# Kernel optimization log

Hardware: AMD Instinct MI355X
Metric: run time of the kernel (lower is better)

The kernel has to match this reference:

```python
import jax, jax.numpy as jnp
import numpy as np

B, T, D = 32, 1024, 512
MAX_LEN = 8192


def setup_inputs() -> dict:
    key = jax.random.key(0)
    k1, k2 = jax.random.split(key)
    x = jax.random.normal(k1, (B, T, D), dtype=jnp.float32)
    duration = jax.random.randint(k2, (B, T), 0, 8, dtype=jnp.int64)
    return {"x": x, "duration": duration, "max_len": MAX_LEN}


def reference(x, duration, max_len):
    # Length regulator: repeat each token vector x[b, i] duration[b, i] times,
    # then zero-pad each batch row to max_len.
    # Equivalent vectorized form: output index j maps to the source token i
    # such that cumsum(duration)[i-1] <= j < cumsum(duration)[i].
    cum = jnp.cumsum(duration, axis=1)                      # [B, T]
    mel_len = cum[:, -1]                                    # [B]
    pos = jnp.arange(max_len)                               # [L]
    # idx[b, j] = searchsorted_right(cum[b], j)
    idx = jax.vmap(lambda c: jnp.searchsorted(c, pos, side="right"))(cum)  # [B, L]
    idx = jnp.minimum(idx, x.shape[1] - 1)
    out = jnp.take_along_axis(x, idx[:, :, None], axis=1)   # [B, L, D]
    mask = (pos[None, :] < mel_len[:, None]).astype(x.dtype)  # [B, L]
    out = out * mask[:, :, None]                            # zero padding region
    return out, mel_len
```

## Files before the change

### kernel.cpp

```cpp
#include <hip/hip_runtime.h>
#include <stdint.h>

#define B_      32
#define T_      1024
#define D_      512
#define MAXLEN_ 8192

typedef float f4 __attribute__((ext_vector_type(4)));

__global__ void lr_scan_idx_kernel(const int* __restrict__ dur,
                                   int* __restrict__ idx,
                                   float* __restrict__ mel_out) {
    int b = blockIdx.x;
    int t = threadIdx.x;
    __shared__ int s[T_];
    s[t] = dur[b * T_ + t];
    __syncthreads();
    #pragma unroll
    for (int off = 1; off < T_; off <<= 1) {
        int v = (t >= off) ? s[t - off] : 0;
        __syncthreads();
        s[t] += v;
        __syncthreads();
    }
    int mel = s[T_ - 1];
    if (t == T_ - 1) {
        mel_out[b] = (float)mel;
    }
    #pragma unroll
    for (int k = 0; k < MAXLEN_ / T_; ++k) {
        int p = t + k * T_;
        int r = -1;
        if (p < mel) {
            int lo = 0, hi = T_;
            #pragma unroll
            for (int it = 0; it < 10; ++it) {
                int mid = (lo + hi) >> 1;
                if (s[mid] <= p) lo = mid + 1; else hi = mid;
            }
            r = lo;
        }
        idx[b * MAXLEN_ + p] = r;
    }
}

__global__ __launch_bounds__(256) void lr_gather_kernel(
        const f4* __restrict__ x,
        const int* __restrict__ idx,
        f4* __restrict__ out) {
    long long gid0 = ((long long)blockIdx.x * blockDim.x + threadIdx.x) * 2;
    int row = (int)(gid0 >> 7);
    int c   = (int)(gid0 & 127);
    int t   = idx[row];
    if (t >= 0) {
        int b = row >> 13;
        const f4* src = x + ((((long long)(b * T_ + t)) << 7) | c);
        out[gid0]     = src[0];
        out[gid0 + 1] = src[1];
    } else {
        f4 z = (f4){0.f, 0.f, 0.f, 0.f};
        out[gid0]     = z;
        out[gid0 + 1] = z;
    }
}

__global__ void lr_cumsum_kernel(const int* __restrict__ dur,
                                 int* __restrict__ cum,
                                 float* __restrict__ mel_out) {
    int b = blockIdx.x;
    int t = threadIdx.x;
    __shared__ int s[T_];
    s[t] = dur[b * T_ + t];
    __syncthreads();
    #pragma unroll
    for (int off = 1; off < T_; off <<= 1) {
        int v = (t >= off) ? s[t - off] : 0;
        __syncthreads();
        s[t] += v;
        __syncthreads();
    }
    cum[b * T_ + t] = s[t];
    if (t == T_ - 1) mel_out[b] = (float)s[t];
}

__global__ void lr_gather_fused_kernel(const f4* __restrict__ x,
                                       const int* __restrict__ cum,
                                       f4* __restrict__ out) {
    const long long total = (long long)B_ * MAXLEN_ * (D_ / 4);
    const long long stride = (long long)gridDim.x * blockDim.x;
    for (long long gid = (long long)blockIdx.x * blockDim.x + threadIdx.x;
         gid < total; gid += stride) {
        int row = (int)(gid >> 7);
        int c   = (int)(gid & 127);
        int b   = row >> 13;
        int p   = row & (MAXLEN_ - 1);
        const int* cm = cum + b * T_;
        int mel = cm[T_ - 1];
        f4 v = (f4){0.f, 0.f, 0.f, 0.f};
        if (p < mel) {
            int lo = 0, hi = T_;
            #pragma unroll
            for (int it = 0; it < 10; ++it) {
                int mid = (lo + hi) >> 1;
                if (cm[mid] <= p) lo = mid + 1; else hi = mid;
            }
            v = x[(((long long)(b * T_ + lo)) << 7) | c];
        }
        out[gid] = v;
    }
}

extern "C" void kernel_launch(void* const* d_in, const int* in_sizes, int n_in,
                              void* d_out, int out_size, void* d_ws, size_t ws_size,
                              hipStream_t stream) {
    const float* x   = (const float*)d_in[0];
    const int*   dur = (const int*)d_in[1];

    float* out     = (float*)d_out;
    float* mel_out = out + (size_t)B_ * MAXLEN_ * D_;

    const size_t need_idx = (size_t)B_ * MAXLEN_ * sizeof(int);

    if (ws_size >= need_idx) {
        int* idx = (int*)d_ws;
        lr_scan_idx_kernel<<<B_, T_, 0, stream>>>(dur, idx, mel_out);
        lr_gather_kernel<<<(B_ * MAXLEN_ * (D_ / 4)) / (256 * 2), 256, 0, stream>>>(
            (const f4*)x, idx, (f4*)out);
    } else {
        int* cum = (int*)d_ws;
        lr_cumsum_kernel<<<B_, T_, 0, stream>>>(dur, cum, mel_out);
        lr_gather_fused_kernel<<<4096, 256, 0, stream>>>((const f4*)x, cum,
                                                         (f4*)out);
    }
}
```

Baseline: 133.7 us.

## Scatter token indices via wave-shuffle scan and regroup gather by output rows

```diff
diff --git a/kernel.cpp b/kernel.cpp
--- a/kernel.cpp
+++ b/kernel.cpp
@@ -8,59 +8,70 @@
 
 typedef float f4 __attribute__((ext_vector_type(4)));
 
-__global__ void lr_scan_idx_kernel(const int* __restrict__ dur,
-                                   int* __restrict__ idx,
-                                   float* __restrict__ mel_out) {
-    int b = blockIdx.x;
-    int t = threadIdx.x;
-    __shared__ int s[T_];
-    s[t] = dur[b * T_ + t];
+__global__ void lr_scan_scatter_kernel(const int* __restrict__ dur,
+                                       int* __restrict__ idx,
+                                       float* __restrict__ mel_out) {
+    int b    = blockIdx.x;
+    int t    = threadIdx.x;
+    int lane = t & 63;
+    int wave = t >> 6;
+
+    int d = dur[b * T_ + t];
+
+    int v = d;
+    #pragma unroll
+    for (int off = 1; off < 64; off <<= 1) {
+        int n = __shfl_up(v, off, 64);
+        if (lane >= off) v += n;
+    }
+
+    __shared__ int wsum[16];
+    if (lane == 63) wsum[wave] = v;
     __syncthreads();
+
+    int off = 0, tot = 0;
     #pragma unroll
-    for (int off = 1; off < T_; off <<= 1) {
-        int v = (t >= off) ? s[t - off] : 0;
-        __syncthreads();
-        s[t] += v;
-        __syncthreads();
+    for (int w = 0; w < 16; ++w) {
+        int s = wsum[w];
+        off += (w < wave) ? s : 0;
+        tot += s;
     }
-    int mel = s[T_ - 1];
-    if (t == T_ - 1) {
-        mel_out[b] = (float)mel;
-    }
-    #pragma unroll
-    for (int k = 0; k < MAXLEN_ / T_; ++k) {
-        int p = t + k * T_;
-        int r = -1;
-        if (p < mel) {
-            int lo = 0, hi = T_;
-            #pragma unroll
-            for (int it = 0; it < 10; ++it) {
-                int mid = (lo + hi) >> 1;
-                if (s[mid] <= p) lo = mid + 1; else hi = mid;
-            }
-            r = lo;
-        }
-        idx[b * MAXLEN_ + p] = r;
-    }
+    int cum  = v + off;
+    int cump = cum - d;
+
+    if (t == T_ - 1) mel_out[b] = (float)tot;
+
+    int* row = idx + b * MAXLEN_;
+    for (int j = cump; j < cum; ++j) row[j] = t;
+    for (int p = tot + t; p < MAXLEN_; p += T_) row[p] = -1;
 }
 
 __global__ __launch_bounds__(256) void lr_gather_kernel(
         const f4* __restrict__ x,
         const int* __restrict__ idx,
         f4* __restrict__ out) {
-    long long gid0 = ((long long)blockIdx.x * blockDim.x + threadIdx.x) * 2;
-    int row = (int)(gid0 >> 7);
-    int c   = (int)(gid0 & 127);
-    int t   = idx[row];
-    if (t >= 0) {
+    unsigned bid   = blockIdx.x;
+    unsigned chunk = gridDim.x >> 3;
+    unsigned nb    = (bid & 7) * chunk + (bid >> 3);
+
+    int row  = (int)(nb * 8) + (int)(threadIdx.x >> 5);
+    int colf = (int)(threadIdx.x & 31);
+    int tt   = idx[row];
+
+    f4* o = out + (((long long)row) << 7) + colf;
+    if (tt >= 0) {
         int b = row >> 13;
-        const f4* src = x + ((((long long)(b * T_ + t)) << 7) | c);
-        out[gid0]     = src[0];
-        out[gid0 + 1] = src[1];
+        const f4* src = x + (((long long)(b * T_ + tt)) << 7) + colf;
+        o[0]  = src[0];
+        o[32] = src[32];
+        o[64] = src[64];
+        o[96] = src[96];
     } else {
         f4 z = (f4){0.f, 0.f, 0.f, 0.f};
-        out[gid0]     = z;
-        out[gid0 + 1] = z;
+        o[0]  = z;
+        o[32] = z;
+        o[64] = z;
+        o[96] = z;
     }
 }
 
@@ -123,8 +134,8 @@
 
     if (ws_size >= need_idx) {
         int* idx = (int*)d_ws;
-        lr_scan_idx_kernel<<<B_, T_, 0, stream>>>(dur, idx, mel_out);
-        lr_gather_kernel<<<(B_ * MAXLEN_ * (D_ / 4)) / (256 * 2), 256, 0, stream>>>(
+        lr_scan_scatter_kernel<<<B_, T_, 0, stream>>>(dur, idx, mel_out);
+        lr_gather_kernel<<<(B_ * MAXLEN_) / 8, 256, 0, stream>>>(
             (const f4*)x, idx, (f4*)out);
     } else {
         int* cum = (int*)d_ws;
```

New measurement: 118.6 us, median of 2. -11.3%, faster.
